# Kernel optimization log

Hardware: AMD Instinct MI355X
Metric: run time of the kernel (lower is better)

The kernel has to match this reference:

```python
import jax, jax.numpy as jnp
import numpy as np

N_NODES = 50000


def gcn_conv(x, edge_index, W, b, n_nodes):
    # PyG GCNConv: add self-loops, symmetric normalization, scatter-add, then bias.
    src = jnp.concatenate([edge_index[0], jnp.arange(n_nodes)])
    dst = jnp.concatenate([edge_index[1], jnp.arange(n_nodes)])
    xw = x @ W  # [N, H]
    deg = jax.ops.segment_sum(jnp.ones_like(dst, dtype=xw.dtype), dst, num_segments=n_nodes)
    dinv = jnp.where(deg > 0, jax.lax.rsqrt(jnp.maximum(deg, 1e-12)), 0.0)
    norm = dinv[src] * dinv[dst]  # [E+N]
    msgs = xw[src] * norm[:, None]  # gather + scale
    out = jax.ops.segment_sum(msgs, dst, num_segments=n_nodes)  # scatter-add
    return out + b


def setup_inputs() -> dict:
    key = jax.random.key(0)
    ks = jax.random.split(key, 12)
    d_in, d_h = 128, 128
    inp = {
        "x": jax.random.normal(ks[0], (N_NODES, d_in), dtype=jnp.float32),
        "edge_index": jax.random.randint(ks[1], (2, 800000), 0, N_NODES, dtype=jnp.int64),
        "conv_W": jax.random.normal(ks[2], (d_in, d_h), dtype=jnp.float32) * 0.05,
        "conv_b": jax.random.normal(ks[3], (d_h,), dtype=jnp.float32) * 0.05,
        "W1": jax.random.normal(ks[4], (d_h, 500), dtype=jnp.float32) * 0.05,
        "b1": jax.random.normal(ks[5], (500,), dtype=jnp.float32) * 0.05,
        "W2": jax.random.normal(ks[6], (500, 500), dtype=jnp.float32) * 0.05,
        "b2": jax.random.normal(ks[7], (500,), dtype=jnp.float32) * 0.05,
        "W3": jax.random.normal(ks[8], (500, 500), dtype=jnp.float32) * 0.05,
        "b3": jax.random.normal(ks[9], (500,), dtype=jnp.float32) * 0.05,
        "Wo": jax.random.normal(ks[10], (500, 1), dtype=jnp.float32) * 0.05,
        "bo": jax.random.normal(ks[11], (1,), dtype=jnp.float32) * 0.05,
    }
    return inp


def reference(x, edge_index, conv_W, conv_b, W1, b1, W2, b2, W3, b3, Wo, bo):
    h = jax.nn.relu(gcn_conv(x, edge_index, conv_W, conv_b, N_NODES))
    h = jax.nn.relu(h @ W1 + b1)
    h = jax.nn.relu(h @ W2 + b2)
    h = jax.nn.relu(h @ W3 + b3)
    return h @ Wo + bo
```

## Files before the change

### kernel.cpp

```cpp
#include <hip/hip_runtime.h>
#include <hip/hip_bf16.h>
#include <hip/hip_fp16.h>

#define NN 50000
#define NE 800000

typedef _Float16 f16;
typedef _Float16 f16x2 __attribute__((ext_vector_type(2)));
typedef _Float16 f16x8 __attribute__((ext_vector_type(8)));
typedef float f32x4 __attribute__((ext_vector_type(4)));

__device__ __forceinline__ void gload16(const f16* g, f16* l) {
    __builtin_amdgcn_global_load_lds(
        (__attribute__((address_space(1))) void*)(void*)g,
        (__attribute__((address_space(3))) void*)(void*)l, 16, 0, 0);
}

__device__ __forceinline__ int detect_mode(const void* ei) {
    const long long* p = (const long long*)ei;
    int ok = 1;
#pragma unroll
    for (int i = 0; i < 8; ++i) {
        long long v = p[i];
        if (v < 0 || v >= NN) ok = 0;
    }
    return ok;
}

__device__ __forceinline__ int edge_at(const void* ei, int mode, int idx) {
    if (mode) return (int)((const long long*)ei)[idx];
    return ((const int*)ei)[idx];
}

#define NBLK 49
__global__ __launch_bounds__(1024)
void scan_blocksum(const int* __restrict__ degi, int* __restrict__ bsum) {
    __shared__ int red[1024];
    int i = blockIdx.x * 1024 + threadIdx.x;
    red[threadIdx.x] = (i < NN) ? degi[i] : 0;
    __syncthreads();
    for (int s = 512; s > 0; s >>= 1) {
        if (threadIdx.x < s) red[threadIdx.x] += red[threadIdx.x + s];
        __syncthreads();
    }
    if (threadIdx.x == 0) bsum[blockIdx.x] = red[0];
}

__global__ __launch_bounds__(1024)
void scan_apply(const int* __restrict__ degi, const int* __restrict__ bsum,
                int* __restrict__ off, float* __restrict__ dinv,
                const float* __restrict__ bo, float* __restrict__ out) {
    __shared__ int tmp[1024];
    __shared__ int base;
    int tid = threadIdx.x;
    if (tid == 0) {
        int a = 0;
        for (int b = 0; b < (int)blockIdx.x; ++b) a += bsum[b];
        base = a;
    }
    int i = blockIdx.x * 1024 + tid;
    int v = (i < NN) ? degi[i] : 0;
    tmp[tid] = v;
    __syncthreads();
    for (int s = 1; s < 1024; s <<= 1) {
        int t = (tid >= s) ? tmp[tid - s] : 0;
        __syncthreads();
        tmp[tid] += t;
        __syncthreads();
    }
    if (i < NN) {
        off[i] = base + tmp[tid] - v;
        dinv[i] = rsqrtf((float)v + 1.0f);
        out[i] = bo[0];
    }
}

__global__ void fill_kernel(const void* ei,
                            const int* __restrict__ off, int* __restrict__ cursor,
                            int* __restrict__ csr) {
    int e = blockIdx.x * blockDim.x + threadIdx.x;
    if (e >= NE) return;
    int mode = detect_mode(ei);
    int s = edge_at(ei, mode, e);
    int d = edge_at(ei, mode, NE + e);
    int pos = atomicAdd(&cursor[d], 1);
    csr[off[d] + pos] = s;
}

__global__ __launch_bounds__(256)
void gather_kernel(const int* __restrict__ csr, const int* __restrict__ off,
                   const int* __restrict__ degi, const f16* __restrict__ xwh,
                   const float* __restrict__ dinv, const float* __restrict__ conv_b,
                   f16* __restrict__ h0h) {
    int wv = threadIdx.x >> 6, lane = threadIdx.x & 63;
    int n = blockIdx.x * 4 + wv;
    if (n >= NN) return;
    int o = off[n], dg = degi[n];
    float ax = 0.f, ay = 0.f, bx = 0.f, by = 0.f;
    int j = 0;
    for (; j + 1 < dg; j += 2) {
        int s0 = csr[o + j], s1 = csr[o + j + 1];
        float d0 = dinv[s0], d1 = dinv[s1];
        f16x2 v0 = *(const f16x2*)(xwh + (size_t)s0 * 128 + lane * 2);
        f16x2 v1 = *(const f16x2*)(xwh + (size_t)s1 * 128 + lane * 2);
        ax += (float)v0[0] * d0; ay += (float)v0[1] * d0;
        bx += (float)v1[0] * d1; by += (float)v1[1] * d1;
    }
    if (j < dg) {
        int s0 = csr[o + j];
        float d0 = dinv[s0];
        f16x2 v0 = *(const f16x2*)(xwh + (size_t)s0 * 128 + lane * 2);
        ax += (float)v0[0] * d0; ay += (float)v0[1] * d0;
    }
    float dn = dinv[n];
    f16x2 vs = *(const f16x2*)(xwh + (size_t)n * 128 + lane * 2);
    float rx = (ax + bx + (float)vs[0] * dn) * dn + conv_b[lane * 2];
    float ry = (ay + by + (float)vs[1] * dn) * dn + conv_b[lane * 2 + 1];
    f16x2 r;
    r[0] = (f16)fmaxf(rx, 0.f);
    r[1] = (f16)fmaxf(ry, 0.f);
    *(f16x2*)(h0h + (size_t)n * 128 + lane * 2) = r;
}

__global__ void prep_all(const float* __restrict__ x, f16* __restrict__ xh,
                         const float* __restrict__ cW, const float* __restrict__ W1,
                         const float* __restrict__ W2, const float* __restrict__ W3,
                         const float* __restrict__ Wo, const float* __restrict__ b1,
                         const float* __restrict__ b2, const float* __restrict__ b3,
                         f16* __restrict__ cWT, f16* __restrict__ W1T,
                         f16* __restrict__ W2T, f16* __restrict__ W3T,
                         float* __restrict__ Wof, float* __restrict__ b1p,
                         float* __restrict__ b2p, float* __restrict__ b3p,
                         const void* ei, int* __restrict__ degi) {
    int i = blockIdx.x * 256 + threadIdx.x;
    if (i < 800000) {
        int e = i * 8;
        float4 u0 = *(const float4*)(x + e);
        float4 u1 = *(const float4*)(x + e + 4);
        f16x8 o;
        o[0] = (f16)u0.x; o[1] = (f16)u0.y; o[2] = (f16)u0.z; o[3] = (f16)u0.w;
        o[4] = (f16)u1.x; o[5] = (f16)u1.y; o[6] = (f16)u1.z; o[7] = (f16)u1.w;
        *(f16x8*)(xh + e) = o;
        return;
    }
    i -= 800000;
    if (i < 16384) { int n = i >> 7, k = i & 127; cWT[i] = (f16)cW[k * 128 + n]; return; }
    i -= 16384;
    if (i < 65536) { int n = i >> 7, k = i & 127; W1T[i] = (f16)((n < 500) ? W1[k * 500 + n] : 0.f); return; }
    i -= 65536;
    if (i < 262144) { int n = i >> 9, k = i & 511; W2T[i] = (f16)((n < 500 && k < 500) ? W2[k * 500 + n] : 0.f); return; }
    i -= 262144;
    if (i < 262144) { int n = i >> 9, k = i & 511; W3T[i] = (f16)((n < 500 && k < 500) ? W3[k * 500 + n] : 0.f); return; }
    i -= 262144;
    if (i < 512) { Wof[i] = (i < 500) ? Wo[i] : 0.f; return; }
    i -= 512;
    if (i < 512) { b1p[i] = (i < 500) ? b1[i] : 0.f; return; }
    i -= 512;
    if (i < 512) { b2p[i] = (i < 500) ? b2[i] : 0.f; return; }
    i -= 512;
    if (i < 512) { b3p[i] = (i < 500) ? b3[i] : 0.f; return; }
    i -= 512;
    if (i < NE) {
        int mode = detect_mode(ei);
        int d = edge_at(ei, mode, NE + i);
        atomicAdd(&degi[d], 1);
    }
}

template <int NT, int BM, int BN, int LOG2WN, bool SWZ, bool RELU, bool BIAS, bool FUSE>
__global__ __launch_bounds__(NT)
void mfma_gemm(const f16* __restrict__ A, const f16* __restrict__ Bt,
               const float* __restrict__ biasp, f16* __restrict__ C,
               const float* __restrict__ Wof, float* __restrict__ out,
               int M, int Npad, int K) {
    constexpr int WN = 1 << LOG2WN;
    constexpr int ASLOTS = BM * 4;
    constexpr int BSLOTS = BN * 4;
    constexpr int LPTA = ASLOTS / NT;
    constexpr int LPTB = BSLOTS / NT;
    constexpr int LPT = LPTA + LPTB;

    int bx, by;
    if (SWZ) {
        int id = blockIdx.x + 2 * blockIdx.y;
        bx = (id >> 3) & 1;
        by = (id >> 4) * 8 + (id & 7);
    } else {
        bx = blockIdx.x; by = blockIdx.y;
    }
    __shared__ f16 As[3][BM * 32];
    __shared__ f16 Bs[3][BN * 32];
    const int tid = threadIdx.x;
    const int lane = tid & 63;
    const int wid = tid >> 6;
    const int wm = wid >> LOG2WN, wn = wid & (WN - 1);
    const int l15 = lane & 15, lk = lane >> 4;
    const int row0 = by * BM, col0 = bx * BN;

    size_t abase[LPTA], bbase[LPTB];
#pragma unroll
    for (int i = 0; i < LPTA; ++i) {
        int s = tid + i * NT;
        int m = s >> 2;
        int kgp = (s & 3) ^ (m & 3) ^ ((m >> 2) & 3);
        int row = row0 + m; if (row > M - 1) row = M - 1;
        abase[i] = (size_t)row * K + kgp * 8;
    }
#pragma unroll
    for (int i = 0; i < LPTB; ++i) {
        int s = tid + i * NT;
        int m = s >> 2;
        int kgp = (s & 3) ^ (m & 3) ^ ((m >> 2) & 3);
        bbase[i] = (size_t)(col0 + m) * K + kgp * 8;
    }
    const int fragoff = l15 * 32 + ((lk ^ (l15 & 3) ^ ((l15 >> 2) & 3)) * 8);
    f32x4 acc[4][4] = {};

    const int nt = K >> 5;

#define STAGE(buf, t)                                                   \
    {                                                                   \
        int _k0 = (t) << 5;                                             \
        _Pragma("unroll")                                               \
        for (int i = 0; i < LPTA; ++i)                                  \
            gload16(A + abase[i] + _k0, &As[buf][(tid + i * NT) * 8]);  \
        _Pragma("unroll")                                               \
        for (int i = 0; i < LPTB; ++i)                                  \
            gload16(Bt + bbase[i] + _k0, &Bs[buf][(tid + i * NT) * 8]); \
    }

#define COMPUTE(buf)                                               \
    {                                                              \
        f16x8 af[4], bf[4];                                        \
        _Pragma("unroll")                                          \
        for (int f = 0; f < 4; ++f) {                              \
            af[f] = *(const f16x8*)&As[buf][(wm * 64 + f * 16) * 32 + fragoff]; \
            bf[f] = *(const f16x8*)&Bs[buf][(wn * 64 + f * 16) * 32 + fragoff]; \
        }                                                          \
        _Pragma("unroll")                                          \
        for (int fi = 0; fi < 4; ++fi)                             \
            _Pragma("unroll")                                      \
            for (int fj = 0; fj < 4; ++fj)                         \
                acc[fi][fj] = __builtin_amdgcn_mfma_f32_16x16x32_f16( \
                    af[fi], bf[fj], acc[fi][fj], 0, 0, 0);         \
    }

    STAGE(0, 0);
    STAGE(1, 1);

    int cur = 0;
    for (int t = 0; t < nt - 2; ++t) {
        int pb = cur + 2; if (pb >= 3) pb -= 3;
        __builtin_amdgcn_sched_barrier(0);
        __builtin_amdgcn_s_barrier();
        __builtin_amdgcn_sched_barrier(0);
        STAGE(pb, t + 2);
        if constexpr (LPT == 4) {
            asm volatile("s_waitcnt vmcnt(8)" ::: "memory");
        } else {
            asm volatile("s_waitcnt vmcnt(6)" ::: "memory");
        }
        __builtin_amdgcn_sched_barrier(0);
        __builtin_amdgcn_s_barrier();
        __builtin_amdgcn_sched_barrier(0);
        COMPUTE(cur);
        cur += 1; if (cur >= 3) cur -= 3;
    }
    {
        __builtin_amdgcn_sched_barrier(0);
        __builtin_amdgcn_s_barrier();
        if constexpr (LPT == 4) {
            asm volatile("s_waitcnt vmcnt(4)" ::: "memory");
        } else {
            asm volatile("s_waitcnt vmcnt(3)" ::: "memory");
        }
        __builtin_amdgcn_sched_barrier(0);
        __builtin_amdgcn_s_barrier();
        __builtin_amdgcn_sched_barrier(0);
        COMPUTE(cur);
        cur += 1; if (cur >= 3) cur -= 3;
    }
    {
        __builtin_amdgcn_sched_barrier(0);
        __builtin_amdgcn_s_barrier();
        asm volatile("s_waitcnt vmcnt(0)" ::: "memory");
        __builtin_amdgcn_sched_barrier(0);
        __builtin_amdgcn_s_barrier();
        __builtin_amdgcn_sched_barrier(0);
        COMPUTE(cur);
    }
#undef STAGE
#undef COMPUTE

    if (FUSE) {
#pragma unroll
        for (int fi = 0; fi < 4; ++fi)
#pragma unroll
            for (int r = 0; r < 4; ++r) {
                float part = 0.f;
#pragma unroll
                for (int fj = 0; fj < 4; ++fj) {
                    int n = col0 + wn * 64 + fj * 16 + l15;
                    float v = acc[fi][fj][r];
                    if (BIAS) v += biasp[n];
                    if (RELU) v = fmaxf(v, 0.f);
                    part += v * Wof[n];
                }
                part += __shfl_xor(part, 1, 64);
                part += __shfl_xor(part, 2, 64);
                part += __shfl_xor(part, 4, 64);
                part += __shfl_xor(part, 8, 64);
                int row = row0 + wm * 64 + fi * 16 + lk * 4 + r;
                if (l15 == 0 && row < M) atomicAdd(out + row, part);
            }
    } else {
#pragma unroll
        for (int fi = 0; fi < 4; ++fi)
#pragma unroll
            for (int r = 0; r < 4; ++r) {
                int row = row0 + wm * 64 + fi * 16 + lk * 4 + r;
                if (row < M) {
#pragma unroll
                    for (int fj = 0; fj < 4; ++fj) {
                        int n = col0 + wn * 64 + fj * 16 + l15;
                        float v = acc[fi][fj][r];
                        if (BIAS) v += biasp[n];
                        if (RELU) v = fmaxf(v, 0.f);
                        C[(size_t)row * Npad + n] = (f16)v;
                    }
                }
            }
    }
}

extern "C" void kernel_launch(void* const* d_in, const int* in_sizes, int n_in,
                              void* d_out, int out_size, void* d_ws, size_t ws_size,
                              hipStream_t stream) {
    const float* x      = (const float*)d_in[0];
    const void*  ei     = d_in[1];
    const float* conv_W = (const float*)d_in[2];
    const float* conv_b = (const float*)d_in[3];
    const float* W1 = (const float*)d_in[4];
    const float* b1 = (const float*)d_in[5];
    const float* W2 = (const float*)d_in[6];
    const float* b2 = (const float*)d_in[7];
    const float* W3 = (const float*)d_in[8];
    const float* b3 = (const float*)d_in[9];
    const float* Wo = (const float*)d_in[10];
    const float* bo = (const float*)d_in[11];
    float* out = (float*)d_out;

    char* ws = (char*)d_ws;
    size_t off_b = 0;
    auto alloc = [&](size_t bytes) {
        void* p = ws + off_b;
        off_b = (off_b + bytes + 255) & ~(size_t)255;
        return p;
    };
    f16*   xh   = (f16*)alloc((size_t)NN * 128 * 2);
    f16*   xwh  = (f16*)alloc((size_t)NN * 128 * 2);
    f16*   h0h  = (f16*)alloc((size_t)NN * 128 * 2);
    f16*   h1h  = (f16*)alloc((size_t)NN * 512 * 2);
    f16*   h2h  = (f16*)alloc((size_t)NN * 512 * 2);
    f16*   cWT  = (f16*)alloc(128 * 128 * 2);
    f16*   W1T  = (f16*)alloc(512 * 128 * 2);
    f16*   W2T  = (f16*)alloc(512 * 512 * 2);
    f16*   W3T  = (f16*)alloc(512 * 512 * 2);
    float* Wof  = (float*)alloc(512 * 4);
    float* b1p  = (float*)alloc(512 * 4);
    float* b2p  = (float*)alloc(512 * 4);
    float* b3p  = (float*)alloc(512 * 4);
    int*   degi   = (int*)alloc(NN * 4);
    int*   offn   = (int*)alloc(NN * 4);
    int*   cursor = (int*)alloc(NN * 4);
    float* dinv   = (float*)alloc(NN * 4);
    int*   bsum   = (int*)alloc(NBLK * 4);
    int*   csr    = (int*)alloc((size_t)NE * 4);

    hipMemsetAsync(degi, 0, (size_t)NN * 4, stream);
    hipMemsetAsync(cursor, 0, (size_t)NN * 4, stream);

    prep_all<<<(2208256 + 255) / 256, 256, 0, stream>>>(
        x, xh, conv_W, W1, W2, W3, Wo, b1, b2, b3,
        cWT, W1T, W2T, W3T, Wof, b1p, b2p, b3p, ei, degi);

    mfma_gemm<256, 128, 128, 1, false, false, false, false>
        <<<dim3(1, 391), 256, 0, stream>>>(
        xh, cWT, nullptr, xwh, nullptr, nullptr, NN, 128, 128);

    scan_blocksum<<<NBLK, 1024, 0, stream>>>(degi, bsum);
    scan_apply<<<NBLK, 1024, 0, stream>>>(degi, bsum, offn, dinv, bo, out);
    fill_kernel<<<(NE + 255) / 256, 256, 0, stream>>>(ei, offn, cursor, csr);
    gather_kernel<<<(NN + 3) / 4, 256, 0, stream>>>(csr, offn, degi, xwh, dinv, conv_b, h0h);

    mfma_gemm<512, 128, 256, 2, true, true, true, false>
        <<<dim3(2, 392), 512, 0, stream>>>(
        h0h, W1T, b1p, h1h, nullptr, nullptr, NN, 512, 128);
    mfma_gemm<512, 128, 256, 2, true, true, true, false>
        <<<dim3(2, 392), 512, 0, stream>>>(
        h1h, W2T, b2p, h2h, nullptr, nullptr, NN, 512, 512);
    mfma_gemm<512, 128, 256, 2, true, true, true, true>
        <<<dim3(2, 392), 512, 0, stream>>>(
        h2h, W3T, b3p, nullptr, Wof, out, NN, 512, 512);
}
```

Measured before the change: 355.6 us.

## Vectorize GCN gather, init cursor from offsets, batch fill edges, raise MFMA priority

The gather kernel now has each wave process four neighbors at once, with every lane loading 8 halves (16 bytes) instead of 2, and reduces the partial sums with cross-lane shuffles. scan_apply sets the cursor to the row offsets, so one memset and the off[] load in fill_kernel go away; each fill thread now handles four edges. The GEMM inner loop raises wave priority around the MFMA block. The changes are meant to cut memory-transaction count and launch or memset overhead, at the cost of shuffle work and idle lanes in the gather tail loop.

```diff
diff --git a/kernel.cpp b/kernel.cpp
--- a/kernel.cpp
+++ b/kernel.cpp
@@ -7,6 +7,7 @@
 
 typedef _Float16 f16;
 typedef _Float16 f16x2 __attribute__((ext_vector_type(2)));
+typedef _Float16 f16x4 __attribute__((ext_vector_type(4)));
 typedef _Float16 f16x8 __attribute__((ext_vector_type(8)));
 typedef float f32x4 __attribute__((ext_vector_type(4)));
 
@@ -48,7 +49,8 @@
 
 __global__ __launch_bounds__(1024)
 void scan_apply(const int* __restrict__ degi, const int* __restrict__ bsum,
-                int* __restrict__ off, float* __restrict__ dinv,
+                int* __restrict__ off, int* __restrict__ cursor,
+                float* __restrict__ dinv,
                 const float* __restrict__ bo, float* __restrict__ out) {
     __shared__ int tmp[1024];
     __shared__ int base;
@@ -69,22 +71,27 @@
         __syncthreads();
     }
     if (i < NN) {
-        off[i] = base + tmp[tid] - v;
+        int o = base + tmp[tid] - v;
+        off[i] = o;
+        cursor[i] = o;
         dinv[i] = rsqrtf((float)v + 1.0f);
         out[i] = bo[0];
     }
 }
 
-__global__ void fill_kernel(const void* ei,
-                            const int* __restrict__ off, int* __restrict__ cursor,
+__global__ void fill_kernel(const void* ei, int* __restrict__ cursor,
                             int* __restrict__ csr) {
-    int e = blockIdx.x * blockDim.x + threadIdx.x;
-    if (e >= NE) return;
+    int gid = blockIdx.x * blockDim.x + threadIdx.x;
+    if (gid >= NE / 4) return;
     int mode = detect_mode(ei);
-    int s = edge_at(ei, mode, e);
-    int d = edge_at(ei, mode, NE + e);
-    int pos = atomicAdd(&cursor[d], 1);
-    csr[off[d] + pos] = s;
+#pragma unroll
+    for (int u = 0; u < 4; ++u) {
+        int e = gid + u * (NE / 4);
+        int s = edge_at(ei, mode, e);
+        int d = edge_at(ei, mode, NE + e);
+        int pos = atomicAdd(&cursor[d], 1);
+        csr[pos] = s;
+    }
 }
 
 __global__ __launch_bounds__(256)
@@ -96,30 +103,45 @@
     int n = blockIdx.x * 4 + wv;
     if (n >= NN) return;
     int o = off[n], dg = degi[n];
-    float ax = 0.f, ay = 0.f, bx = 0.f, by = 0.f;
+    int q = lane >> 4;
+    int fl = (lane & 15) * 8;
+    float acc[8] = {};
     int j = 0;
-    for (; j + 1 < dg; j += 2) {
-        int s0 = csr[o + j], s1 = csr[o + j + 1];
-        float d0 = dinv[s0], d1 = dinv[s1];
-        f16x2 v0 = *(const f16x2*)(xwh + (size_t)s0 * 128 + lane * 2);
-        f16x2 v1 = *(const f16x2*)(xwh + (size_t)s1 * 128 + lane * 2);
-        ax += (float)v0[0] * d0; ay += (float)v0[1] * d0;
-        bx += (float)v1[0] * d1; by += (float)v1[1] * d1;
-    }
-    if (j < dg) {
-        int s0 = csr[o + j];
-        float d0 = dinv[s0];
-        f16x2 v0 = *(const f16x2*)(xwh + (size_t)s0 * 128 + lane * 2);
-        ax += (float)v0[0] * d0; ay += (float)v0[1] * d0;
-    }
-    float dn = dinv[n];
-    f16x2 vs = *(const f16x2*)(xwh + (size_t)n * 128 + lane * 2);
-    float rx = (ax + bx + (float)vs[0] * dn) * dn + conv_b[lane * 2];
-    float ry = (ay + by + (float)vs[1] * dn) * dn + conv_b[lane * 2 + 1];
-    f16x2 r;
-    r[0] = (f16)fmaxf(rx, 0.f);
-    r[1] = (f16)fmaxf(ry, 0.f);
-    *(f16x2*)(h0h + (size_t)n * 128 + lane * 2) = r;
+    for (; j + 8 <= dg; j += 8) {
+        int sa = csr[o + j + q];
+        int sb = csr[o + j + 4 + q];
+        float da = dinv[sa], db = dinv[sb];
+        f16x8 va = *(const f16x8*)(xwh + (size_t)sa * 128 + fl);
+        f16x8 vb = *(const f16x8*)(xwh + (size_t)sb * 128 + fl);
+#pragma unroll
+        for (int k = 0; k < 8; ++k)
+            acc[k] += (float)va[k] * da + (float)vb[k] * db;
+    }
+    for (; j < dg; ++j) {
+        if ((j & 3) == q) {
+            int s = csr[o + j];
+            float d = dinv[s];
+            f16x8 v = *(const f16x8*)(xwh + (size_t)s * 128 + fl);
+#pragma unroll
+            for (int k = 0; k < 8; ++k) acc[k] += (float)v[k] * d;
+        }
+    }
+#pragma unroll
+    for (int k = 0; k < 8; ++k) {
+        acc[k] += __shfl_xor(acc[k], 16, 64);
+        acc[k] += __shfl_xor(acc[k], 32, 64);
+    }
+    if (q == 0) {
+        float dn = dinv[n];
+        f16x8 vs = *(const f16x8*)(xwh + (size_t)n * 128 + fl);
+        f16x8 r;
+#pragma unroll
+        for (int k = 0; k < 8; ++k) {
+            float rv = (acc[k] + (float)vs[k] * dn) * dn + conv_b[fl + k];
+            r[k] = (f16)fmaxf(rv, 0.f);
+        }
+        *(f16x8*)(h0h + (size_t)n * 128 + fl) = r;
+    }
 }
 
 __global__ void prep_all(const float* __restrict__ x, f16* __restrict__ xh,
@@ -237,12 +259,14 @@
             af[f] = *(const f16x8*)&As[buf][(wm * 64 + f * 16) * 32 + fragoff]; \
             bf[f] = *(const f16x8*)&Bs[buf][(wn * 64 + f * 16) * 32 + fragoff]; \
         }                                                          \
+        __builtin_amdgcn_s_setprio(1);                             \
         _Pragma("unroll")                                          \
         for (int fi = 0; fi < 4; ++fi)                             \
             _Pragma("unroll")                                      \
             for (int fj = 0; fj < 4; ++fj)                         \
                 acc[fi][fj] = __builtin_amdgcn_mfma_f32_16x16x32_f16( \
                     af[fi], bf[fj], acc[fi][fj], 0, 0, 0);         \
+        __builtin_amdgcn_s_setprio(0);                             \
     }
 
     STAGE(0, 0);
@@ -378,7 +402,6 @@
     int*   csr    = (int*)alloc((size_t)NE * 4);
 
     hipMemsetAsync(degi, 0, (size_t)NN * 4, stream);
-    hipMemsetAsync(cursor, 0, (size_t)NN * 4, stream);
 
     prep_all<<<(2208256 + 255) / 256, 256, 0, stream>>>(
         x, xh, conv_W, W1, W2, W3, Wo, b1, b2, b3,
@@ -389,8 +412,8 @@
         xh, cWT, nullptr, xwh, nullptr, nullptr, NN, 128, 128);
 
     scan_blocksum<<<NBLK, 1024, 0, stream>>>(degi, bsum);
-    scan_apply<<<NBLK, 1024, 0, stream>>>(degi, bsum, offn, dinv, bo, out);
-    fill_kernel<<<(NE + 255) / 256, 256, 0, stream>>>(ei, offn, cursor, csr);
+    scan_apply<<<NBLK, 1024, 0, stream>>>(degi, bsum, offn, cursor, dinv, bo, out);
+    fill_kernel<<<(NE / 4 + 255) / 256, 256, 0, stream>>>(ei, cursor, csr);
     gather_kernel<<<(NN + 3) / 4, 256, 0, stream>>>(csr, offn, degi, xwh, dinv, conv_b, h0h);
 
     mfma_gemm<512, 128, 256, 2, true, true, true, false>
```

Result: slower. 380.2 us (+6.9%).
